# Kernel tuning notes

Measured on AMD Instinct MI355X. Metric: run time of the kernel, lower is better.

The kernel has to match this reference:

```python
import jax, jax.numpy as jnp
import numpy as np

EPS = 0.0  # GINConv eps

def _gin_conv(x, edge_index, W1, b1, W2, b2, n_nodes):
    # GINConv: mlp((1+eps)*x + sum_{j in N(i)} x_j)
    src, dst = edge_index[0], edge_index[1]
    agg = jax.ops.segment_sum(x[src], dst, num_segments=n_nodes)  # [N, d]
    h = (1.0 + EPS) * x + agg
    h = jax.nn.relu(h @ W1 + b1)  # Linear -> Identity(BN off) -> ReLU
    return h @ W2 + b2            # second Linear


def setup_inputs() -> dict:
    key = jax.random.key(0)
    ks = jax.random.split(key, 10)
    N, E = 50000, 600000
    d_in, d_hid, d_out = 128, 256, 128
    x = jax.random.normal(ks[0], (N, d_in), dtype=jnp.float32)
    edge_index = jax.random.randint(ks[1], (2, E), 0, N, dtype=jnp.int64)

    def lin(k, fan_in, fan_out):
        bound = 1.0 / np.sqrt(fan_in)
        kw, kb = jax.random.split(k)
        W = jax.random.uniform(kw, (fan_in, fan_out), jnp.float32, -bound, bound)
        b = jax.random.uniform(kb, (fan_out,), jnp.float32, -bound, bound)
        return W, b

    W1a, b1a = lin(ks[2], d_in, d_hid)   # conv0 mlp: 128->256
    W2a, b2a = lin(ks[3], d_hid, d_hid)  # conv0 mlp: 256->256
    W1b, b1b = lin(ks[4], d_hid, d_hid)  # conv1 mlp: 256->256
    W2b, b2b = lin(ks[5], d_hid, d_out)  # conv1 mlp: 256->128
    return {"x": x, "W1a": W1a, "b1a": b1a, "W2a": W2a, "b2a": b2a,
            "W1b": W1b, "b1b": b1b, "W2b": W2b, "b2b": b2b,
            "edge_index": edge_index}


def reference(x, W1a, b1a, W2a, b2a, W1b, b1b, W2b, b2b, edge_index):
    n_nodes = x.shape[0]
    # layer 0: GINConv -> relu (use_bn=False; dropout is identity in eval)
    h = _gin_conv(x, edge_index, W1a, b1a, W2a, b2a, n_nodes)
    h = jax.nn.relu(h)
    # final GINConv (no activation after, per forward())
    return _gin_conv(h, edge_index, W1b, b1b, W2b, b2b, n_nodes)
```

## Files before the change

kernel.cpp:

```cpp
#include <hip/hip_runtime.h>


typedef __bf16 bf16x8 __attribute__((ext_vector_type(8)));
typedef float f32x4 __attribute__((ext_vector_type(4)));
typedef unsigned short u16x8 __attribute__((ext_vector_type(8)));
typedef unsigned short u16x4 __attribute__((ext_vector_type(4)));
typedef unsigned int uint32;

__device__ __forceinline__ unsigned short f2bf(float f) {
  uint32 u = __builtin_bit_cast(uint32, f);
  u += 0x7FFFu + ((u >> 16) & 1u);
  return (unsigned short)(u >> 16);
}
__device__ __forceinline__ float bf2f(unsigned short h) {
  return __builtin_bit_cast(float, (uint32)h << 16);
}

#define G2L16(gp, lp)                                                        \
  __builtin_amdgcn_global_load_lds(                                          \
      (const __attribute__((address_space(1))) void*)(gp),                   \
      (__attribute__((address_space(3))) void*)(lp), 16, 0, 0)

__global__ void hist(const int* __restrict__ eidx, int* __restrict__ deg, int E) {
  int e = blockIdx.x * blockDim.x + threadIdx.x;
  if (e < E) atomicAdd(&deg[eidx[e + E]], 1);
}

__global__ __launch_bounds__(256) void block_sums(const int* __restrict__ deg,
                                                  int* __restrict__ bsum, int Nn) {
  __shared__ int sm[256];
  int t = threadIdx.x;
  int i = blockIdx.x * 256 + t;
  sm[t] = (i < Nn) ? deg[i] : 0;
  __syncthreads();
#pragma unroll
  for (int off = 128; off > 0; off >>= 1) {
    if (t < off) sm[t] += sm[t + off];
    __syncthreads();
  }
  if (t == 0) bsum[blockIdx.x] = sm[0];
}

__global__ __launch_bounds__(256) void scan_bsums(int* __restrict__ bsum, int nb) {
  __shared__ int sm[256];
  int t = threadIdx.x;
  int v = (t < nb) ? bsum[t] : 0;
  sm[t] = v;
  __syncthreads();
#pragma unroll
  for (int off = 1; off < 256; off <<= 1) {
    int add = (t >= off) ? sm[t - off] : 0;
    __syncthreads();
    sm[t] += add;
    __syncthreads();
  }
  if (t < nb) bsum[t] = sm[t] - v;
}

__global__ __launch_bounds__(256) void block_scan(const int* __restrict__ deg,
                                                  const int* __restrict__ bsum,
                                                  int* __restrict__ offs,
                                                  int* __restrict__ pos, int Nn) {
  __shared__ int sm[256];
  int t = threadIdx.x;
  int i = blockIdx.x * 256 + t;
  int v = (i < Nn) ? deg[i] : 0;
  sm[t] = v;
  __syncthreads();
#pragma unroll
  for (int off = 1; off < 256; off <<= 1) {
    int add = (t >= off) ? sm[t - off] : 0;
    __syncthreads();
    sm[t] += add;
    __syncthreads();
  }
  int ex = bsum[blockIdx.x] + sm[t] - v;
  if (i < Nn) {
    offs[i] = ex;
    pos[i] = ex;
    if (i == Nn - 1) offs[Nn] = ex + v;
  }
}

__global__ void fill_csr(const int* __restrict__ eidx, int* __restrict__ pos,
                         int* __restrict__ esrc, int E) {
  int e = blockIdx.x * blockDim.x + threadIdx.x;
  if (e < E) {
    int s = eidx[e];
    int d = eidx[e + E];
    int p = atomicAdd(&pos[d], 1);
    esrc[p] = s;
  }
}

__global__ __launch_bounds__(256) void prep(
    int* __restrict__ deg, int Nn,
    const float* __restrict__ x, unsigned short* __restrict__ xb, long long n4,
    const float* __restrict__ W1a, const float* __restrict__ W2a,
    const float* __restrict__ W1b, const float* __restrict__ W2b,
    unsigned short* __restrict__ w1t, unsigned short* __restrict__ w2t,
    unsigned short* __restrict__ w3t, unsigned short* __restrict__ w4t) {
  int zb = (Nn + 255) >> 8;
  int b = blockIdx.x;
  int t = threadIdx.x;
  if (b < zb) {
    int i = b * 256 + t;
    if (i < Nn) deg[i] = 0;
  } else if (b < zb + 768) {
    int i = (b - zb) * 256 + t;
    const float* W;
    unsigned short* WT;
    int K, N, j;
    if (i < 32768) {
      W = W1a; WT = w1t; K = 128; N = 256; j = i;
    } else if (i < 98304) {
      W = W2a; WT = w2t; K = 256; N = 256; j = i - 32768;
    } else if (i < 163840) {
      W = W1b; WT = w3t; K = 256; N = 256; j = i - 98304;
    } else {
      W = W2b; WT = w4t; K = 256; N = 128; j = i - 163840;
    }
    int k = j / N, n = j - k * N;
    WT[n * K + k] = f2bf(W[j]);
  } else {
    long long i = (long long)(b - zb - 768) * 256 + t;
    long long stride = (long long)(gridDim.x - zb - 768) * 256;
    for (; i < n4; i += stride) {
      float4 v = ((const float4*)x)[i];
      u16x4 o;
      o.x = f2bf(v.x); o.y = f2bf(v.y); o.z = f2bf(v.z); o.w = f2bf(v.w);
      ((u16x4*)xb)[i] = o;
    }
  }
}

__global__ __launch_bounds__(256) void agg_bf16_128(
    unsigned short* __restrict__ out, const unsigned short* __restrict__ xb,
    const int* __restrict__ offs, const int* __restrict__ esrc, int Nn) {
  int node = blockIdx.x * 4 + (threadIdx.x >> 6);
  if (node >= Nn) return;
  int lane = threadIdx.x & 63;
  int sub = lane >> 4, l16 = lane & 15;
  int beg = offs[node], end = offs[node + 1];
  int total = end - beg + 1;
  const unsigned short* xp = xb + l16 * 8;
  float acc[8] = {};
  for (int j0 = 0; j0 < total; j0 += 8) {
#pragma unroll
    for (int u = 0; u < 2; ++u) {
      int j = j0 + u * 4 + sub;
      int rv = esrc[beg + j - (j > 0)];
      long long row = (j > 0 && j < total) ? rv : node;
      float sel = (j < total) ? 1.f : 0.f;
      u16x8 v = *(const u16x8*)(xp + row * 128);
#pragma unroll
      for (int k = 0; k < 8; ++k)
        acc[k] = fmaf(bf2f(v[k]), sel, acc[k]);
    }
  }
#pragma unroll
  for (int k = 0; k < 8; ++k) acc[k] += __shfl_xor(acc[k], 16);
#pragma unroll
  for (int k = 0; k < 8; ++k) acc[k] += __shfl_xor(acc[k], 32);
  if (sub == 0) {
    u16x8 o;
#pragma unroll
    for (int k = 0; k < 8; ++k) o[k] = f2bf(acc[k]);
    *(u16x8*)(out + (long long)node * 128 + l16 * 8) = o;
  }
}

__global__ __launch_bounds__(256) void agg_bf16_256(
    unsigned short* __restrict__ out, const unsigned short* __restrict__ h,
    const int* __restrict__ offs, const int* __restrict__ esrc, int Nn) {
  int node = blockIdx.x * 4 + (threadIdx.x >> 6);
  if (node >= Nn) return;
  int lane = threadIdx.x & 63;
  int sub = lane >> 5, l32 = lane & 31;
  int beg = offs[node], end = offs[node + 1];
  int total = end - beg + 1;
  const unsigned short* hp = h + l32 * 8;
  float acc[8] = {};
  for (int j0 = 0; j0 < total; j0 += 8) {
#pragma unroll
    for (int u = 0; u < 4; ++u) {
      int j = j0 + u * 2 + sub;
      int rv = esrc[beg + j - (j > 0)];
      long long row = (j > 0 && j < total) ? rv : node;
      float sel = (j < total) ? 1.f : 0.f;
      u16x8 v = *(const u16x8*)(hp + row * 256);
#pragma unroll
      for (int k = 0; k < 8; ++k)
        acc[k] = fmaf(bf2f(v[k]), sel, acc[k]);
    }
  }
#pragma unroll
  for (int k = 0; k < 8; ++k) acc[k] += __shfl_xor(acc[k], 32);
  if (sub == 0) {
    u16x8 o;
#pragma unroll
    for (int k = 0; k < 8; ++k) o[k] = f2bf(acc[k]);
    *(u16x8*)(out + (long long)node * 256 + l32 * 8) = o;
  }
}

template <bool RELU, bool OUT_BF16>
__global__ __launch_bounds__(256) void gemm_mfma(
    const unsigned short* __restrict__ A, const unsigned short* __restrict__ BT,
    const float* __restrict__ bias, void* __restrict__ C, int M, int K, int N) {
  __shared__ unsigned short As[128 * 32];
  __shared__ unsigned short Bs[128 * 32];
  const int tid = threadIdx.x;
  const int wave = tid >> 6, lane = tid & 63;
  const int wm = wave & 1, wn = wave >> 1;
  const int quad = lane >> 4, l16 = lane & 15;
  const int rowBase = blockIdx.y * 128;
  const int colBase = blockIdx.x * 128;

  const int srow = wave * 32 + (lane >> 2);
  const int koff = (lane & 3) * 8;
  long long ra0 = min(rowBase + srow, M - 1);
  long long ra1 = min(rowBase + srow + 16, M - 1);
  const unsigned short* ga0 = A + ra0 * K + koff;
  const unsigned short* ga1 = A + ra1 * K + koff;
  const unsigned short* gb0 = BT + (long long)(colBase + srow) * K + koff;
  const unsigned short* gb1 = BT + (long long)(colBase + srow + 16) * K + koff;
  unsigned short* la0 = As + wave * 1024;
  unsigned short* la1 = As + wave * 1024 + 512;
  unsigned short* lb0 = Bs + wave * 1024;
  unsigned short* lb1 = Bs + wave * 1024 + 512;

  f32x4 acc[4][4] = {};

  for (int k0 = 0; k0 < K; k0 += 32) {
    G2L16(ga0, la0);
    G2L16(ga1, la1);
    G2L16(gb0, lb0);
    G2L16(gb1, lb1);
    ga0 += 32; ga1 += 32; gb0 += 32; gb1 += 32;
    __syncthreads();

    bf16x8 af[4], bfr[4];
    const int arow = wm * 64 + l16;
    const int brow = wn * 64 + l16;
#pragma unroll
    for (int mi = 0; mi < 4; ++mi)
      af[mi] = *(const bf16x8*)(As + (arow + mi * 16) * 32 + quad * 8);
#pragma unroll
    for (int ni = 0; ni < 4; ++ni)
      bfr[ni] = *(const bf16x8*)(Bs + (brow + ni * 16) * 32 + quad * 8);
#pragma unroll
    for (int mi = 0; mi < 4; ++mi)
#pragma unroll
      for (int ni = 0; ni < 4; ++ni)
        acc[mi][ni] = __builtin_amdgcn_mfma_f32_16x16x32_bf16(
            af[mi], bfr[ni], acc[mi][ni], 0, 0, 0);
    __syncthreads();
  }

  float bias_v[4];
#pragma unroll
  for (int ni = 0; ni < 4; ++ni)
    bias_v[ni] = bias[colBase + wn * 64 + ni * 16 + l16];
#pragma unroll
  for (int mi = 0; mi < 4; ++mi) {
#pragma unroll
    for (int r = 0; r < 4; ++r) {
      int row = rowBase + wm * 64 + mi * 16 + quad * 4 + r;
      if (row < M) {
#pragma unroll
        for (int ni = 0; ni < 4; ++ni) {
          float o = acc[mi][ni][r] + bias_v[ni];
          if (RELU) o = fmaxf(o, 0.f);
          int col = colBase + wn * 64 + ni * 16 + l16;
          if (OUT_BF16)
            ((unsigned short*)C)[(long long)row * N + col] = f2bf(o);
          else
            ((float*)C)[(long long)row * N + col] = o;
        }
      }
    }
  }
}

extern "C" void kernel_launch(void* const* d_in, const int* in_sizes, int n_in,
                              void* d_out, int out_size, void* d_ws, size_t ws_size,
                              hipStream_t stream) {
  const float* x   = (const float*)d_in[0];
  const float* W1a = (const float*)d_in[1];
  const float* b1a = (const float*)d_in[2];
  const float* W2a = (const float*)d_in[3];
  const float* b2a = (const float*)d_in[4];
  const float* W1b = (const float*)d_in[5];
  const float* b1b = (const float*)d_in[6];
  const float* W2b = (const float*)d_in[7];
  const float* b2b = (const float*)d_in[8];
  const int*   ei  = (const int*)d_in[9];

  const int Nn = in_sizes[0] / 128;
  const int E  = in_sizes[9] / 2;
  float* out = (float*)d_out;

  unsigned short* t   = (unsigned short*)d_ws;
  unsigned short* h   = t  + (size_t)Nn * 256;
  unsigned short* g0  = h  + (size_t)Nn * 256;
  unsigned short* g1  = g0 + (size_t)Nn * 128;
  unsigned short* t2  = g1 + (size_t)Nn * 256;
  unsigned short* xb  = t2 + (size_t)Nn * 256;
  unsigned short* w1t = xb + (size_t)Nn * 128;
  unsigned short* w2t = w1t + 256 * 128;
  unsigned short* w3t = w2t + 256 * 256;
  unsigned short* w4t = w3t + 256 * 256;
  int* deg  = (int*)(w4t + 128 * 256);
  int* offs = deg + Nn;
  int* pos  = offs + Nn + 1;
  int* esrc = pos + Nn;
  int* bsum = esrc + E;

  dim3 blk(256);
  int nb = (Nn + 255) / 256;

  prep<<<nb + 768 + 2048, blk, 0, stream>>>(deg, Nn, x, xb,
                                            (long long)Nn * 128 / 4,
                                            W1a, W2a, W1b, W2b,
                                            w1t, w2t, w3t, w4t);
  hist<<<(E + 255) / 256, blk, 0, stream>>>(ei, deg, E);
  block_sums<<<nb, blk, 0, stream>>>(deg, bsum, Nn);
  scan_bsums<<<1, blk, 0, stream>>>(bsum, nb);
  block_scan<<<nb, blk, 0, stream>>>(deg, bsum, offs, pos, Nn);
  fill_csr<<<(E + 255) / 256, blk, 0, stream>>>(ei, pos, esrc, E);

  int aggBlocks = (Nn + 3) / 4;
  int gy = (Nn + 127) / 128;

  agg_bf16_128<<<aggBlocks, blk, 0, stream>>>(g0, xb, offs, esrc, Nn);
  gemm_mfma<true, true><<<dim3(2, gy), blk, 0, stream>>>(g0, w1t, b1a, t, Nn, 128, 256);
  gemm_mfma<true, true><<<dim3(2, gy), blk, 0, stream>>>(t, w2t, b2a, h, Nn, 256, 256);

  agg_bf16_256<<<aggBlocks, blk, 0, stream>>>(g1, h, offs, esrc, Nn);
  gemm_mfma<true, true><<<dim3(2, gy), blk, 0, stream>>>(g1, w3t, b1b, t2, Nn, 256, 256);
  gemm_mfma<false, false><<<dim3(1, gy), blk, 0, stream>>>(t2, w4t, b2b, out, Nn, 256, 128);
}
```

Before: 312.1 us.

## Fuse each GIN MLP's two GEMMs into one kernel via LDS intermediate

Replaces the pair of separate MFMA GEMM launches per GIN layer with a single fused kernel. Each block computes a 64-row tile of the hidden activation, keeps it in LDS as bf16, and then multiplies it by the second weight matrix. This removes the global write and read of the N×256 intermediate and two kernel launches. It also doubles the unroll of the gather loops in both aggregation kernels to put more loads in flight. In exchange, each block uses more LDS (about 50KB) and recomputes full-width weight tiles per 64-row block, which may lower occupancy and increase weight traffic.

Result: faster. 294.0 us (-5.8%).

```diff
diff --git a/kernel.cpp b/kernel.cpp
--- a/kernel.cpp
+++ b/kernel.cpp
@@ -145,9 +145,9 @@
   int total = end - beg + 1;
   const unsigned short* xp = xb + l16 * 8;
   float acc[8] = {};
-  for (int j0 = 0; j0 < total; j0 += 8) {
-#pragma unroll
-    for (int u = 0; u < 2; ++u) {
+  for (int j0 = 0; j0 < total; j0 += 16) {
+#pragma unroll
+    for (int u = 0; u < 4; ++u) {
       int j = j0 + u * 4 + sub;
       int rv = esrc[beg + j - (j > 0)];
       long long row = (j > 0 && j < total) ? rv : node;
@@ -181,9 +181,9 @@
   int total = end - beg + 1;
   const unsigned short* hp = h + l32 * 8;
   float acc[8] = {};
-  for (int j0 = 0; j0 < total; j0 += 8) {
-#pragma unroll
-    for (int u = 0; u < 4; ++u) {
+  for (int j0 = 0; j0 < total; j0 += 16) {
+#pragma unroll
+    for (int u = 0; u < 8; ++u) {
       int j = j0 + u * 2 + sub;
       int rv = esrc[beg + j - (j > 0)];
       long long row = (j > 0 && j < total) ? rv : node;
@@ -204,51 +204,42 @@
   }
 }
 
-template <bool RELU, bool OUT_BF16>
-__global__ __launch_bounds__(256) void gemm_mfma(
-    const unsigned short* __restrict__ A, const unsigned short* __restrict__ BT,
-    const float* __restrict__ bias, void* __restrict__ C, int M, int K, int N) {
-  __shared__ unsigned short As[128 * 32];
-  __shared__ unsigned short Bs[128 * 32];
+template <int K1, int N2, bool OUT_BF16>
+__global__ __launch_bounds__(256) void fused_mlp(
+    const unsigned short* __restrict__ A,
+    const unsigned short* __restrict__ BT1, const float* __restrict__ b1,
+    const unsigned short* __restrict__ BT2, const float* __restrict__ b2,
+    void* __restrict__ Cout, int M) {
+  __shared__ unsigned short As[64 * 32];
+  __shared__ unsigned short Bs[256 * 32];
+  __shared__ unsigned short Ts[64 * 264];
   const int tid = threadIdx.x;
   const int wave = tid >> 6, lane = tid & 63;
-  const int wm = wave & 1, wn = wave >> 1;
   const int quad = lane >> 4, l16 = lane & 15;
-  const int rowBase = blockIdx.y * 128;
-  const int colBase = blockIdx.x * 128;
-
-  const int srow = wave * 32 + (lane >> 2);
-  const int koff = (lane & 3) * 8;
-  long long ra0 = min(rowBase + srow, M - 1);
-  long long ra1 = min(rowBase + srow + 16, M - 1);
-  const unsigned short* ga0 = A + ra0 * K + koff;
-  const unsigned short* ga1 = A + ra1 * K + koff;
-  const unsigned short* gb0 = BT + (long long)(colBase + srow) * K + koff;
-  const unsigned short* gb1 = BT + (long long)(colBase + srow + 16) * K + koff;
-  unsigned short* la0 = As + wave * 1024;
-  unsigned short* la1 = As + wave * 1024 + 512;
-  unsigned short* lb0 = Bs + wave * 1024;
-  unsigned short* lb1 = Bs + wave * 1024 + 512;
-
+  const int rowBase = blockIdx.x * 64;
+  const int r16 = lane >> 2;
+  const int kq = lane & 3;
+
+  long long arow = min(rowBase + wave * 16 + r16, M - 1);
+  const unsigned short* ga = A + arow * K1 + kq * 8;
+  const unsigned short* gb = BT1 + (long long)(wave * 64 + r16) * K1 + kq * 8;
+  unsigned short* la = As + wave * 16 * 32;
   f32x4 acc[4][4] = {};
-
-  for (int k0 = 0; k0 < K; k0 += 32) {
-    G2L16(ga0, la0);
-    G2L16(ga1, la1);
-    G2L16(gb0, lb0);
-    G2L16(gb1, lb1);
-    ga0 += 32; ga1 += 32; gb0 += 32; gb1 += 32;
-    __syncthreads();
-
+  for (int k0 = 0; k0 < K1; k0 += 32) {
+    G2L16(ga, la);
+    ga += 32;
+#pragma unroll
+    for (int c = 0; c < 4; ++c)
+      G2L16(gb + (long long)(16 * c) * K1, Bs + (wave * 64 + 16 * c) * 32);
+    gb += 32;
+    __syncthreads();
     bf16x8 af[4], bfr[4];
-    const int arow = wm * 64 + l16;
-    const int brow = wn * 64 + l16;
-#pragma unroll
-    for (int mi = 0; mi < 4; ++mi)
-      af[mi] = *(const bf16x8*)(As + (arow + mi * 16) * 32 + quad * 8);
+#pragma unroll
+    for (int mi = 0; mi < 4; ++mi)
+      af[mi] = *(const bf16x8*)(As + (mi * 16 + l16) * 32 + quad * 8);
 #pragma unroll
     for (int ni = 0; ni < 4; ++ni)
-      bfr[ni] = *(const bf16x8*)(Bs + (brow + ni * 16) * 32 + quad * 8);
+      bfr[ni] = *(const bf16x8*)(Bs + (wave * 64 + ni * 16 + l16) * 32 + quad * 8);
 #pragma unroll
     for (int mi = 0; mi < 4; ++mi)
 #pragma unroll
@@ -257,29 +248,62 @@
             af[mi], bfr[ni], acc[mi][ni], 0, 0, 0);
     __syncthreads();
   }
-
-  float bias_v[4];
-#pragma unroll
-  for (int ni = 0; ni < 4; ++ni)
-    bias_v[ni] = bias[colBase + wn * 64 + ni * 16 + l16];
-#pragma unroll
-  for (int mi = 0; mi < 4; ++mi) {
-#pragma unroll
-    for (int r = 0; r < 4; ++r) {
-      int row = rowBase + wm * 64 + mi * 16 + quad * 4 + r;
-      if (row < M) {
-#pragma unroll
-        for (int ni = 0; ni < 4; ++ni) {
-          float o = acc[mi][ni][r] + bias_v[ni];
-          if (RELU) o = fmaxf(o, 0.f);
-          int col = colBase + wn * 64 + ni * 16 + l16;
+#pragma unroll
+  for (int ni = 0; ni < 4; ++ni) {
+    int col = wave * 64 + ni * 16 + l16;
+    float bv = b1[col];
+#pragma unroll
+    for (int mi = 0; mi < 4; ++mi)
+#pragma unroll
+      for (int r = 0; r < 4; ++r) {
+        int row = mi * 16 + quad * 4 + r;
+        Ts[row * 264 + col] = f2bf(fmaxf(acc[mi][ni][r] + bv, 0.f));
+      }
+  }
+  __syncthreads();
+
+  constexpr int NI2 = N2 / 64;
+  const int wcol = wave * (N2 / 4);
+  const unsigned short* gb2 = BT2 + (long long)(wcol + r16) * 256 + kq * 8;
+  f32x4 acc2[4][NI2] = {};
+  for (int k2 = 0; k2 < 256; k2 += 32) {
+#pragma unroll
+    for (int c = 0; c < NI2; ++c)
+      G2L16(gb2 + (long long)(16 * c) * 256, Bs + (wcol + 16 * c) * 32);
+    gb2 += 32;
+    __syncthreads();
+    bf16x8 af[4], bfr[NI2];
+#pragma unroll
+    for (int mi = 0; mi < 4; ++mi)
+      af[mi] = *(const bf16x8*)(Ts + (mi * 16 + l16) * 264 + k2 + quad * 8);
+#pragma unroll
+    for (int ni = 0; ni < NI2; ++ni)
+      bfr[ni] = *(const bf16x8*)(Bs + (wcol + ni * 16 + l16) * 32 + quad * 8);
+#pragma unroll
+    for (int mi = 0; mi < 4; ++mi)
+#pragma unroll
+      for (int ni = 0; ni < NI2; ++ni)
+        acc2[mi][ni] = __builtin_amdgcn_mfma_f32_16x16x32_bf16(
+            af[mi], bfr[ni], acc2[mi][ni], 0, 0, 0);
+    __syncthreads();
+  }
+#pragma unroll
+  for (int ni = 0; ni < NI2; ++ni) {
+    int col = wcol + ni * 16 + l16;
+    float bv = b2[col];
+#pragma unroll
+    for (int mi = 0; mi < 4; ++mi)
+#pragma unroll
+      for (int r = 0; r < 4; ++r) {
+        int row = rowBase + mi * 16 + quad * 4 + r;
+        if (row < M) {
+          float o = acc2[mi][ni][r] + bv;
           if (OUT_BF16)
-            ((unsigned short*)C)[(long long)row * N + col] = f2bf(o);
+            ((unsigned short*)Cout)[(long long)row * N2 + col] = f2bf(fmaxf(o, 0.f));
           else
-            ((float*)C)[(long long)row * N + col] = o;
+            ((float*)Cout)[(long long)row * N2 + col] = o;
         }
       }
-    }
   }
 }
 
@@ -301,12 +325,10 @@
   const int E  = in_sizes[9] / 2;
   float* out = (float*)d_out;
 
-  unsigned short* t   = (unsigned short*)d_ws;
-  unsigned short* h   = t  + (size_t)Nn * 256;
+  unsigned short* h   = (unsigned short*)d_ws;
   unsigned short* g0  = h  + (size_t)Nn * 256;
   unsigned short* g1  = g0 + (size_t)Nn * 128;
-  unsigned short* t2  = g1 + (size_t)Nn * 256;
-  unsigned short* xb  = t2 + (size_t)Nn * 256;
+  unsigned short* xb  = g1 + (size_t)Nn * 256;
   unsigned short* w1t = xb + (size_t)Nn * 128;
   unsigned short* w2t = w1t + 256 * 128;
   unsigned short* w3t = w2t + 256 * 256;
@@ -331,13 +353,13 @@
   fill_csr<<<(E + 255) / 256, blk, 0, stream>>>(ei, pos, esrc, E);
 
   int aggBlocks = (Nn + 3) / 4;
-  int gy = (Nn + 127) / 128;
+  int mlpBlocks = (Nn + 63) / 64;
 
   agg_bf16_128<<<aggBlocks, blk, 0, stream>>>(g0, xb, offs, esrc, Nn);
-  gemm_mfma<true, true><<<dim3(2, gy), blk, 0, stream>>>(g0, w1t, b1a, t, Nn, 128, 256);
-  gemm_mfma<true, true><<<dim3(2, gy), blk, 0, stream>>>(t, w2t, b2a, h, Nn, 256, 256);
+  fused_mlp<128, 256, true><<<mlpBlocks, blk, 0, stream>>>(
+      g0, w1t, b1a, w2t, b2a, h, Nn);
 
   agg_bf16_256<<<aggBlocks, blk, 0, stream>>>(g1, h, offs, esrc, Nn);
-  gemm_mfma<true, true><<<dim3(2, gy), blk, 0, stream>>>(g1, w3t, b1b, t2, Nn, 256, 256);
-  gemm_mfma<false, false><<<dim3(1, gy), blk, 0, stream>>>(t2, w4t, b2b, out, Nn, 256, 128);
-}
+  fused_mlp<256, 128, false><<<mlpBlocks, blk, 0, stream>>>(
+      g1, w3t, b1b, w4t, b2b, out, Nn);
+}
```
